# Performance work log

Measured on AMD Instinct MI355X. Metric: run time of the kernel, lower is better.

## Reference

```python
import jax, jax.numpy as jnp
import numpy as np

UNITS = 1024
HEADS = 16
DEPTH = UNITS // HEADS          # 64
REL_LEN = 64 + 1                # max_relative_position + 1
M = 2 * REL_LEN - 1             # 129 relative buckets (bidirectional)
B, L = 4, 1024


def setup_inputs() -> dict:
    key = jax.random.key(0)
    ks = jax.random.split(key, 8)
    s = 0.02
    x = jax.random.normal(ks[0], (B, L, UNITS), jnp.float32)
    wq = jax.random.normal(ks[1], (UNITS, UNITS), jnp.float32) * s
    wk = jax.random.normal(ks[2], (UNITS, UNITS), jnp.float32) * s
    wv = jax.random.normal(ks[3], (UNITS, UNITS), jnp.float32) * s
    wo = jax.random.normal(ks[4], (UNITS, UNITS), jnp.float32) * s
    bo = jnp.zeros((UNITS,), jnp.float32)
    ek = jax.random.normal(ks[5], (HEADS, M, DEPTH), jnp.float32) * s
    ev = jax.random.normal(ks[6], (HEADS, M, DEPTH), jnp.float32) * s
    pad_mask = jnp.zeros((B, 1, 1, L), jnp.float32)  # 1.0 where padded
    return dict(x=x, pad_mask=pad_mask, wq=wq, wk=wk, wv=wv, wo=wo, bo=bo, ek=ek, ev=ev)


def _rel_idx(length):
    # relative offset j - i, clipped to [-(REL_LEN-1), REL_LEN-1], shifted to [0, M-1].
    # Equivalent to the pad/reshape/slice skew trick: padding_relative_embeddings tiles the
    # edge embeddings (== clipping) and relative_to_absolute_pos realizes idx = j - i + REL_LEN - 1.
    i = jnp.arange(length)
    off = i[None, :] - i[:, None]
    return jnp.clip(off, -(REL_LEN - 1), REL_LEN - 1) + (REL_LEN - 1)  # [L, L] int32


def _forward(x, pad_mask, wq, wk, wv, wo, bo, ek, ev):
    b, length, _ = x.shape

    def split_heads(h):  # [B, L, U] -> [B, H, L, D]
        return jnp.transpose(h.reshape(b, length, HEADS, DEPTH), (0, 2, 1, 3))

    q = split_heads(x @ wq)
    k = split_heads(x @ wk)
    v = split_heads(x @ wv)

    idx = _rel_idx(length)                                   # [L, L]
    qk = jnp.einsum('bhid,bhjd->bhij', q, k)                 # [B, H, L, L]
    # relative key logits: q . E_k over relative buckets, then relative->absolute gather
    qm = jnp.einsum('bhld,hmd->bhlm', q, ek)                 # [B, H, L, M]
    rel_k = jnp.take_along_axis(qm, idx[None, None, :, :], axis=-1)  # [B, H, L, L]
    logits = (qk + rel_k) / jnp.sqrt(jnp.asarray(DEPTH, jnp.float32))
    logits = logits + pad_mask * -1e9
    attn = jax.nn.softmax(logits, axis=-1)                   # [B, H, L, L]
    out = jnp.einsum('bhij,bhjd->bhid', attn, v)             # [B, H, L, D]

    # value relative position: out[b,h,i,d] += sum_j attn[b,h,i,j] * E_v[h, idx[i,j], d]
    # Implemented by scattering attn into relative buckets (avoids the [H,L,L,D] tensor
    # the original materializes), mathematically identical.
    def per_query(attn_i, idx_i):  # attn_i [B, H, L], idx_i [L]
        return jax.ops.segment_sum(jnp.moveaxis(attn_i, -1, 0), idx_i, num_segments=M)  # [M, B, H]

    wr = jax.vmap(per_query, in_axes=(2, 0))(attn, idx)      # [L, M, B, H]
    wr = jnp.transpose(wr, (2, 3, 0, 1))                     # [B, H, L, M]
    out = out + jnp.einsum('bhlm,hmd->bhld', wr, ev)

    out = jnp.transpose(out, (0, 2, 1, 3)).reshape(b, length, UNITS)  # combine heads
    return out @ wo + bo


def reference(x, pad_mask, wq, wk, wv, wo, bo, ek, ev):
    return _forward(x, pad_mask, wq, wk, wv, wo, bo, ek, ev)
```

## Files before the change

kernel.cpp:

```cpp
#include <hip/hip_runtime.h>

typedef unsigned short u16;
typedef short s16x8 __attribute__((ext_vector_type(8)));
typedef float f32x4 __attribute__((ext_vector_type(4)));

static __device__ __forceinline__ u16 f2b(float f) {
  union { float f; unsigned u; } v; v.f = f;
  unsigned r = v.u + 0x7fffu + ((v.u >> 16) & 1u);
  return (u16)(r >> 16);
}
static __device__ __forceinline__ float b2f(u16 u) {
  union { unsigned u; float f; } v; v.u = ((unsigned)u) << 16;
  return v.f;
}

#define MFMA16(a, b, c) __builtin_amdgcn_mfma_f32_16x16x32_bf16((a), (b), (c), 0, 0, 0)

static __device__ __forceinline__ void gload_lds16(const u16* g, u16* l) {
  __builtin_amdgcn_global_load_lds((const __attribute__((address_space(1))) void*)g,
                                   (__attribute__((address_space(3))) void*)l, 16, 0, 0);
}

__global__ void k_cast_x(const float* __restrict__ src, u16* __restrict__ dst, int n4) {
  int i = blockIdx.x * blockDim.x + threadIdx.x;
  if (i >= n4) return;
  float4 v = ((const float4*)src)[i];
  ushort4 o;
  o.x = f2b(v.x); o.y = f2b(v.y); o.z = f2b(v.z); o.w = f2b(v.w);
  ((ushort4*)dst)[i] = o;
}

__global__ void k_transpose_w(const float* wq, const float* wk, const float* wv, const float* wo,
                              u16* dq, u16* dk, u16* dv, u16* dwo) {
  const float* src; u16* dst;
  int z = blockIdx.z;
  if (z == 0)      { src = wq; dst = dq; }
  else if (z == 1) { src = wk; dst = dk; }
  else if (z == 2) { src = wv; dst = dv; }
  else             { src = wo; dst = dwo; }
  __shared__ float t[32][33];
  int x0 = blockIdx.x * 32, y0 = blockIdx.y * 32;
  int tx = threadIdx.x, ty = threadIdx.y;
#pragma unroll
  for (int k = 0; k < 4; k++) t[ty + 8 * k][tx] = src[(size_t)(y0 + ty + 8 * k) * 1024 + x0 + tx];
  __syncthreads();
#pragma unroll
  for (int k = 0; k < 4; k++) dst[(size_t)(x0 + ty + 8 * k) * 1024 + y0 + tx] = f2b(t[tx][ty + 8 * k]);
}

__global__ void k_prep_rel(const float* __restrict__ ek, const float* __restrict__ ev,
                           u16* __restrict__ ekb, u16* __restrict__ evt) {
  int i = blockIdx.x * blockDim.x + threadIdx.x;
  if (i < 16 * 144 * 64) {
    int h = i / (144 * 64); int rem = i % (144 * 64); int m = rem / 64; int d = rem % 64;
    ekb[i] = (m < 129) ? f2b(ek[((size_t)h * 129 + m) * 64 + d]) : (u16)0;
  }
  if (i < 16 * 64 * 160) {
    int h = i / (64 * 160); int rem = i % (64 * 160); int d = rem / 160; int mm = rem % 160;
    evt[i] = (mm < 129) ? f2b(ev[((size_t)h * 129 + mm) * 64 + d]) : (u16)0;
  }
}

template <int MODE>
static __device__ __forceinline__ void gemm_body(const u16* __restrict__ A, const u16* __restrict__ Bt,
                                                 void* __restrict__ Cout, const float* __restrict__ bias,
                                                 int bx, int by) {
  __shared__ u16 As[128 * 32];
  __shared__ u16 Bs[128 * 32];
  int tid = threadIdx.x;
  int w = tid >> 6, lane = tid & 63;
  int wrw = w >> 1, wcw = w & 1, lr = lane & 15, lk = lane >> 4;
  int m0 = by * 128, n0 = bx * 128;
  f32x4 acc[4][4] = {};
  int crow = lane >> 2;
  int ccol = (lane & 3) * 8;
  const u16* gA = &A [(size_t)(m0 + w * 32 + crow) * 1024 + ccol];
  const u16* gB = &Bt[(size_t)(n0 + w * 32 + crow) * 1024 + ccol];
  u16* lA = &As[w * 32 * 32];
  u16* lB = &Bs[w * 32 * 32];
  for (int k0 = 0; k0 < 1024; k0 += 32) {
    __syncthreads();
    gload_lds16(gA + k0,             lA);
    gload_lds16(gA + k0 + 16 * 1024, lA + 16 * 32);
    gload_lds16(gB + k0,             lB);
    gload_lds16(gB + k0 + 16 * 1024, lB + 16 * 32);
    __syncthreads();
    s16x8 af[4], bfr[4];
#pragma unroll
    for (int mt = 0; mt < 4; mt++) af[mt]  = *(const s16x8*)&As[(wrw * 64 + mt * 16 + lr) * 32 + lk * 8];
#pragma unroll
    for (int nt = 0; nt < 4; nt++) bfr[nt] = *(const s16x8*)&Bs[(wcw * 64 + nt * 16 + lr) * 32 + lk * 8];
    __builtin_amdgcn_s_setprio(1);
#pragma unroll
    for (int mt = 0; mt < 4; mt++)
#pragma unroll
      for (int nt = 0; nt < 4; nt++) {
        if (MODE == 1) acc[mt][nt] = MFMA16(bfr[nt], af[mt], acc[mt][nt]);
        else           acc[mt][nt] = MFMA16(af[mt], bfr[nt], acc[mt][nt]);
      }
    __builtin_amdgcn_s_setprio(0);
  }
#pragma unroll
  for (int mt = 0; mt < 4; mt++)
#pragma unroll
    for (int nt = 0; nt < 4; nt++)
#pragma unroll
      for (int r = 0; r < 4; r++) {
        float v = acc[mt][nt][r];
        if (MODE == 1) {
          int u = n0 + wcw * 64 + nt * 16 + lk * 4 + r;
          int l = m0 + wrw * 64 + mt * 16 + lr;
          int bb = l >> 10, ll = l & 1023;
          int hh = u >> 6, dd = u & 63;
          ((u16*)Cout)[((size_t)(bb * 16 + hh)) * 65536 + (size_t)dd * 1024 + ll] = f2b(v);
        } else {
          int row = m0 + wrw * 64 + mt * 16 + lk * 4 + r;
          int col = n0 + wcw * 64 + nt * 16 + lr;
          if (MODE == 2) {
            ((float*)Cout)[(size_t)row * 1024 + col] = v + bias[col];
          } else {
            int bb = row >> 10, l = row & 1023;
            int hh = col >> 6, dd = col & 63;
            ((u16*)Cout)[((size_t)(bb * 16 + hh)) * 65536 + (size_t)l * 64 + dd] = f2b(v);
          }
        }
      }
}

__global__ __launch_bounds__(256) void k_gemm_qk(const u16* __restrict__ A,
                                                 const u16* __restrict__ BtQ, const u16* __restrict__ BtK,
                                                 u16* __restrict__ Qo, u16* __restrict__ Ko) {
  const u16* Bt = blockIdx.z ? BtK : BtQ;
  u16* C        = blockIdx.z ? Ko  : Qo;
  gemm_body<0>(A, Bt, C, nullptr, blockIdx.x, blockIdx.y);
}
__global__ __launch_bounds__(256) void k_gemm_v(const u16* __restrict__ A, const u16* __restrict__ Bt,
                                                u16* __restrict__ Vo) {
  gemm_body<1>(A, Bt, Vo, nullptr, blockIdx.x, blockIdx.y);
}
__global__ __launch_bounds__(256) void k_gemm_out(const u16* __restrict__ A, const u16* __restrict__ Bt,
                                                  float* __restrict__ Cout, const float* __restrict__ bias) {
  gemm_body<2>(A, Bt, Cout, bias, blockIdx.x, blockIdx.y);
}

__global__ __launch_bounds__(64) void k_attn(const u16* __restrict__ Qg, const u16* __restrict__ Kg,
                                             const u16* __restrict__ Vt, const u16* __restrict__ ekb,
                                             const u16* __restrict__ evt, const float* __restrict__ pmask,
                                             u16* __restrict__ Og) {
  __shared__ alignas(16) char smem[16128];
  u16* qm_s   = (u16*)smem;
  u16* P_s    = (u16*)(smem + 4352);
  u16* wrb    = (u16*)(smem + 8704);
  u16* mask_s = (u16*)(smem + 14080);

  int lane = threadIdx.x;
  int lr = lane & 15, lk = lane >> 4;
  int wg = (blockIdx.x & 7) * 512 + (blockIdx.x >> 3);
  int bh = wg >> 6, it = wg & 63;
  int b = bh >> 4, h = bh & 15;
  int i0 = it * 16;

  {
    const float4* pm4 = (const float4*)(pmask + (size_t)b * 1024);
#pragma unroll
    for (int t = 0; t < 4; t++) {
      float4 v = pm4[lane * 4 + t];
      unsigned w0 = (unsigned)f2b(v.x * -1e9f) | ((unsigned)f2b(v.y * -1e9f) << 16);
      unsigned w1 = (unsigned)f2b(v.z * -1e9f) | ((unsigned)f2b(v.w * -1e9f) << 16);
      ((unsigned*)mask_s)[lane * 8 + t * 2]     = w0;
      ((unsigned*)mask_s)[lane * 8 + t * 2 + 1] = w1;
    }
  }
  for (int t = lane; t < 1344; t += 64) ((unsigned*)wrb)[t] = 0u;

  const u16* qp = &Qg[((size_t)bh * 1024 + i0 + lr) * 64 + lk * 8];
  s16x8 aq0 = *(const s16x8*)qp;
  s16x8 aq1 = *(const s16x8*)(qp + 32);

#pragma unroll
  for (int nt = 0; nt < 9; nt++) {
    f32x4 c = {};
    const u16* ekp = &ekb[((size_t)h * 144 + nt * 16 + lr) * 64 + lk * 8];
    c = MFMA16(aq0, *(const s16x8*)ekp, c);
    c = MFMA16(aq1, *(const s16x8*)(ekp + 32), c);
    int mcol = nt * 16 + lr;
    if (mcol < 129) {
#pragma unroll
      for (int r = 0; r < 4; r++) qm_s[(lk * 4 + r) * 136 + mcol] = f2b(c[r]);
    }
  }

  float ssum = 0.f, lsum = 0.f, rsum = 0.f;
  f32x4 oacc[4] = {};
  const int ig = i0 + lr;

  for (int jt = 0; jt < 8; jt++) {
    int j0 = jt * 128;
    float p[8][4];
    const u16* kbase = &Kg[((size_t)bh * 1024 + j0 + lr) * 64 + lk * 8];
#pragma unroll
    for (int nt = 0; nt < 8; nt++) {
      f32x4 c = {};
      const u16* kp = kbase + nt * 16 * 64;
      c = MFMA16(*(const s16x8*)kp, aq0, c);
      c = MFMA16(*(const s16x8*)(kp + 32), aq1, c);
#pragma unroll
      for (int r = 0; r < 4; r++) {
        int j = j0 + nt * 16 + lk * 4 + r;
        int dl = j - ig;
        dl = dl < -64 ? -64 : (dl > 64 ? 64 : dl);
        float qmv = b2f(qm_s[lr * 136 + dl + 64]);
        float madd = b2f(mask_s[j]);
        float sval = fminf((c[r] + qmv) * 0.125f + madd, 80.f);
        float pv = __expf(sval);
        p[nt][r] = pv;
        ssum += pv;
      }
    }
#pragma unroll
    for (int nt = 0; nt < 8; nt++) {
      unsigned lo, hi;
      asm("v_cvt_pk_bf16_f32 %0, %1, %2" : "=v"(lo) : "v"(p[nt][0]), "v"(p[nt][1]));
      asm("v_cvt_pk_bf16_f32 %0, %1, %2" : "=v"(hi) : "v"(p[nt][2]), "v"(p[nt][3]));
      uint2 pk; pk.x = lo; pk.y = hi;
      *(uint2*)&P_s[lr * 136 + nt * 16 + lk * 4] = pk;
    }
    __builtin_amdgcn_s_setprio(1);
    {
      s16x8 ap[4];
#pragma unroll
      for (int kk = 0; kk < 4; kk++) ap[kk] = *(const s16x8*)&P_s[lr * 136 + kk * 32 + lk * 8];
      const u16* vbase = &Vt[((size_t)bh * 64 + lr) * 1024 + j0 + lk * 8];
#pragma unroll
      for (int nt = 0; nt < 4; nt++) {
        const u16* vp = vbase + nt * 16 * 1024;
#pragma unroll
        for (int kk = 0; kk < 4; kk++)
          oacc[nt] = MFMA16(ap[kk], *(const s16x8*)(vp + kk * 32), oacc[nt]);
      }
    }
    __builtin_amdgcn_s_setprio(0);
    {
      int jmin = j0 + lk * 4;
      int jmax = j0 + 112 + lk * 4 + 3;
      if (jmax <= ig - 64) {
        float s = 0.f;
#pragma unroll
        for (int nt = 0; nt < 8; nt++) s += (p[nt][0] + p[nt][1]) + (p[nt][2] + p[nt][3]);
        lsum += s;
      } else if (jmin >= ig + 64) {
        float s = 0.f;
#pragma unroll
        for (int nt = 0; nt < 8; nt++) s += (p[nt][0] + p[nt][1]) + (p[nt][2] + p[nt][3]);
        rsum += s;
      } else {
#pragma unroll
        for (int nt = 0; nt < 8; nt++)
#pragma unroll
          for (int r = 0; r < 4; r++) {
            int dl = j0 + nt * 16 + lk * 4 + r - ig;
            if (dl <= -64) lsum += p[nt][r];
            else if (dl >= 64) rsum += p[nt][r];
            else wrb[lr * 168 + dl + 64] = f2b(p[nt][r]);
          }
      }
    }
  }

  lsum += __shfl_xor(lsum, 16); lsum += __shfl_xor(lsum, 32);
  rsum += __shfl_xor(rsum, 16); rsum += __shfl_xor(rsum, 32);
  ssum += __shfl_xor(ssum, 16); ssum += __shfl_xor(ssum, 32);
  if (lk == 0) {
    wrb[lr * 168]       = f2b(lsum);
    wrb[lr * 168 + 128] = f2b(rsum);
  }

  __builtin_amdgcn_s_setprio(1);
  {
    s16x8 aw[5];
#pragma unroll
    for (int kk = 0; kk < 5; kk++) aw[kk] = *(const s16x8*)&wrb[lr * 168 + kk * 32 + lk * 8];
    const u16* ebase = &evt[((size_t)h * 64 + lr) * 160 + lk * 8];
#pragma unroll
    for (int nt = 0; nt < 4; nt++) {
      const u16* ep = ebase + nt * 16 * 160;
#pragma unroll
      for (int kk = 0; kk < 5; kk++)
        oacc[nt] = MFMA16(aw[kk], *(const s16x8*)(ep + kk * 32), oacc[nt]);
    }
  }
  __builtin_amdgcn_s_setprio(0);

  float rden[4];
#pragma unroll
  for (int r = 0; r < 4; r++) rden[r] = 1.0f / __shfl(ssum, lk * 4 + r);
  u16* obase = &Og[((size_t)(b * 1024 + i0)) * 1024 + h * 64];
#pragma unroll
  for (int nt = 0; nt < 4; nt++)
#pragma unroll
    for (int r = 0; r < 4; r++) {
      int il = lk * 4 + r;
      obase[(size_t)il * 1024 + nt * 16 + lr] = f2b(oacc[nt][r] * rden[r]);
    }
}

#define OFF_XB   0u
#define OFF_WQT  8388608u
#define OFF_WKT  10485760u
#define OFF_WVT  12582912u
#define OFF_WOT  14680064u
#define OFF_Q    16777216u
#define OFF_K    25165824u
#define OFF_VT   33554432u
#define OFF_O    41943040u
#define OFF_EKB  50331648u
#define OFF_EVT  50626560u

extern "C" void kernel_launch(void* const* d_in, const int* in_sizes, int n_in,
                              void* d_out, int out_size, void* d_ws, size_t ws_size,
                              hipStream_t stream) {
  const float* x  = (const float*)d_in[0];
  const float* pm = (const float*)d_in[1];
  const float* wq = (const float*)d_in[2];
  const float* wk = (const float*)d_in[3];
  const float* wv = (const float*)d_in[4];
  const float* wo = (const float*)d_in[5];
  const float* bo = (const float*)d_in[6];
  const float* ek = (const float*)d_in[7];
  const float* ev = (const float*)d_in[8];
  char* ws = (char*)d_ws;
  u16* Xb  = (u16*)(ws + OFF_XB);
  u16* Wqt = (u16*)(ws + OFF_WQT);
  u16* Wkt = (u16*)(ws + OFF_WKT);
  u16* Wvt = (u16*)(ws + OFF_WVT);
  u16* Wot = (u16*)(ws + OFF_WOT);
  u16* Qg  = (u16*)(ws + OFF_Q);
  u16* Kg  = (u16*)(ws + OFF_K);
  u16* Vtg = (u16*)(ws + OFF_VT);
  u16* Og  = (u16*)(ws + OFF_O);
  u16* EKB = (u16*)(ws + OFF_EKB);
  u16* EVT = (u16*)(ws + OFF_EVT);

  k_cast_x<<<4096, 256, 0, stream>>>(x, Xb, 1048576);
  {
    dim3 tb(32, 8), tg(32, 32, 4);
    k_transpose_w<<<tg, tb, 0, stream>>>(wq, wk, wv, wo, Wqt, Wkt, Wvt, Wot);
  }
  k_prep_rel<<<640, 256, 0, stream>>>(ek, ev, EKB, EVT);
  {
    dim3 gqk(8, 32, 2);
    k_gemm_qk<<<gqk, 256, 0, stream>>>(Xb, Wqt, Wkt, Qg, Kg);
    dim3 gv(8, 32);
    k_gemm_v<<<gv, 256, 0, stream>>>(Xb, Wvt, Vtg);
    k_attn<<<4096, 64, 0, stream>>>(Qg, Kg, Vtg, EKB, EVT, pm, Og);
    dim3 go(8, 32);
    k_gemm_out<<<go, 256, 0, stream>>>(Og, Wot, (float*)d_out, bo);
  }
}
```

Before: 319.7 us.

## Specialize attention tiles by relative region, fold scale into Q, double-buffer GEMM

Attention key tiles are split into left-clipped, diagonal and right-clipped classes, so the far tiles skip the per-element relative-logit lookups and bucket scatter and use a single per-row clipped value. The softmax scale and log2(e) are folded into the Q projection output so the kernel can use a raw hardware exp2. The pad mask is precomputed once in bf16 instead of per block. The right-edge value bucket is applied as a scalar FMA instead of an extra MFMA K-step. The projection GEMMs gain double-buffered LDS loads. The costs are more code paths and extra bf16 rounding of the scaled Q.

After: 338.2 us. 1.06x slower.

```diff
diff --git a/kernel.cpp b/kernel.cpp
--- a/kernel.cpp
+++ b/kernel.cpp
@@ -3,6 +3,9 @@
 typedef unsigned short u16;
 typedef short s16x8 __attribute__((ext_vector_type(8)));
 typedef float f32x4 __attribute__((ext_vector_type(4)));
+
+#define ALPHA 0.18033688f
+#define MASKC -1.44269504e9f
 
 static __device__ __forceinline__ u16 f2b(float f) {
   union { float f; unsigned u; } v; v.f = f;
@@ -12,6 +15,9 @@
 static __device__ __forceinline__ float b2f(u16 u) {
   union { unsigned u; float f; } v; v.u = ((unsigned)u) << 16;
   return v.f;
+}
+static __device__ __forceinline__ float exp2_hw(float x) {
+  float r; asm("v_exp_f32 %0, %1" : "=v"(r) : "v"(x)); return r;
 }
 
 #define MFMA16(a, b, c) __builtin_amdgcn_mfma_f32_16x16x32_bf16((a), (b), (c), 0, 0, 0)
@@ -49,7 +55,8 @@
 }
 
 __global__ void k_prep_rel(const float* __restrict__ ek, const float* __restrict__ ev,
-                           u16* __restrict__ ekb, u16* __restrict__ evt) {
+                           const float* __restrict__ pm,
+                           u16* __restrict__ ekb, u16* __restrict__ evt, u16* __restrict__ maskb) {
   int i = blockIdx.x * blockDim.x + threadIdx.x;
   if (i < 16 * 144 * 64) {
     int h = i / (144 * 64); int rem = i % (144 * 64); int m = rem / 64; int d = rem % 64;
@@ -59,14 +66,15 @@
     int h = i / (64 * 160); int rem = i % (64 * 160); int d = rem / 160; int mm = rem % 160;
     evt[i] = (mm < 129) ? f2b(ev[((size_t)h * 129 + mm) * 64 + d]) : (u16)0;
   }
+  if (i < 4096) maskb[i] = f2b(pm[i] * MASKC);
 }
 
 template <int MODE>
 static __device__ __forceinline__ void gemm_body(const u16* __restrict__ A, const u16* __restrict__ Bt,
                                                  void* __restrict__ Cout, const float* __restrict__ bias,
-                                                 int bx, int by) {
-  __shared__ u16 As[128 * 32];
-  __shared__ u16 Bs[128 * 32];
+                                                 float oscale, int bx, int by) {
+  __shared__ u16 As[2][128 * 32];
+  __shared__ u16 Bs[2][128 * 32];
   int tid = threadIdx.x;
   int w = tid >> 6, lane = tid & 63;
   int wrw = w >> 1, wcw = w & 1, lr = lane & 15, lk = lane >> 4;
@@ -76,20 +84,26 @@
   int ccol = (lane & 3) * 8;
   const u16* gA = &A [(size_t)(m0 + w * 32 + crow) * 1024 + ccol];
   const u16* gB = &Bt[(size_t)(n0 + w * 32 + crow) * 1024 + ccol];
-  u16* lA = &As[w * 32 * 32];
-  u16* lB = &Bs[w * 32 * 32];
-  for (int k0 = 0; k0 < 1024; k0 += 32) {
-    __syncthreads();
+
+  auto STAGE = [&](int buf, int k0) {
+    u16* lA = &As[buf][w * 1024];
+    u16* lB = &Bs[buf][w * 1024];
     gload_lds16(gA + k0,             lA);
     gload_lds16(gA + k0 + 16 * 1024, lA + 16 * 32);
     gload_lds16(gB + k0,             lB);
     gload_lds16(gB + k0 + 16 * 1024, lB + 16 * 32);
-    __syncthreads();
+  };
+
+  STAGE(0, 0);
+  __syncthreads();
+  int cur = 0;
+  for (int t = 0; t < 32; t++) {
+    if (t < 31) STAGE(cur ^ 1, (t + 1) * 32);
     s16x8 af[4], bfr[4];
 #pragma unroll
-    for (int mt = 0; mt < 4; mt++) af[mt]  = *(const s16x8*)&As[(wrw * 64 + mt * 16 + lr) * 32 + lk * 8];
-#pragma unroll
-    for (int nt = 0; nt < 4; nt++) bfr[nt] = *(const s16x8*)&Bs[(wcw * 64 + nt * 16 + lr) * 32 + lk * 8];
+    for (int mt = 0; mt < 4; mt++) af[mt]  = *(const s16x8*)&As[cur][(wrw * 64 + mt * 16 + lr) * 32 + lk * 8];
+#pragma unroll
+    for (int nt = 0; nt < 4; nt++) bfr[nt] = *(const s16x8*)&Bs[cur][(wcw * 64 + nt * 16 + lr) * 32 + lk * 8];
     __builtin_amdgcn_s_setprio(1);
 #pragma unroll
     for (int mt = 0; mt < 4; mt++)
@@ -99,6 +113,8 @@
         else           acc[mt][nt] = MFMA16(af[mt], bfr[nt], acc[mt][nt]);
       }
     __builtin_amdgcn_s_setprio(0);
+    __syncthreads();
+    cur ^= 1;
   }
 #pragma unroll
   for (int mt = 0; mt < 4; mt++)
@@ -121,7 +137,7 @@
           } else {
             int bb = row >> 10, l = row & 1023;
             int hh = col >> 6, dd = col & 63;
-            ((u16*)Cout)[((size_t)(bb * 16 + hh)) * 65536 + (size_t)l * 64 + dd] = f2b(v);
+            ((u16*)Cout)[((size_t)(bb * 16 + hh)) * 65536 + (size_t)l * 64 + dd] = f2b(v * oscale);
           }
         }
       }
@@ -132,26 +148,101 @@
                                                  u16* __restrict__ Qo, u16* __restrict__ Ko) {
   const u16* Bt = blockIdx.z ? BtK : BtQ;
   u16* C        = blockIdx.z ? Ko  : Qo;
-  gemm_body<0>(A, Bt, C, nullptr, blockIdx.x, blockIdx.y);
+  gemm_body<0>(A, Bt, C, nullptr, blockIdx.z ? 1.0f : ALPHA, blockIdx.x, blockIdx.y);
 }
 __global__ __launch_bounds__(256) void k_gemm_v(const u16* __restrict__ A, const u16* __restrict__ Bt,
                                                 u16* __restrict__ Vo) {
-  gemm_body<1>(A, Bt, Vo, nullptr, blockIdx.x, blockIdx.y);
+  gemm_body<1>(A, Bt, Vo, nullptr, 1.0f, blockIdx.x, blockIdx.y);
 }
 __global__ __launch_bounds__(256) void k_gemm_out(const u16* __restrict__ A, const u16* __restrict__ Bt,
                                                   float* __restrict__ Cout, const float* __restrict__ bias) {
-  gemm_body<2>(A, Bt, Cout, bias, blockIdx.x, blockIdx.y);
+  gemm_body<2>(A, Bt, Cout, bias, 1.0f, blockIdx.x, blockIdx.y);
+}
+
+template <int CLS>
+static __device__ __forceinline__ void attn_tile(
+    int j0, const u16* __restrict__ Kt, const u16* __restrict__ Vt0, const u16* __restrict__ mrow,
+    s16x8 aq0, s16x8 aq1, u16* qm_s, u16* P_s, u16* wrb,
+    float qmL, float qmR, int lr, int lk, int ig,
+    f32x4 oacc[4], float& ssum, float& lsum, float& rsum)
+{
+  float p[8][4];
+  const u16* kbase = Kt + (size_t)(j0 + lr) * 64 + lk * 8;
+  const u16* mbase = &mrow[j0 + lk * 4];
+#pragma unroll
+  for (int nt = 0; nt < 8; nt++) {
+    f32x4 c = {};
+    const u16* kp = kbase + nt * 1024;
+    c = MFMA16(*(const s16x8*)kp, aq0, c);
+    c = MFMA16(*(const s16x8*)(kp + 32), aq1, c);
+    ushort4 mv = *(const ushort4*)(mbase + nt * 16);
+#pragma unroll
+    for (int r = 0; r < 4; r++) {
+      float qmv;
+      if (CLS == 0) qmv = qmL;
+      else if (CLS == 2) qmv = qmR;
+      else {
+        int dl = j0 + nt * 16 + lk * 4 + r - ig;
+        dl = dl < -64 ? -64 : (dl > 64 ? 64 : dl);
+        qmv = b2f(qm_s[lr * 136 + dl + 64]);
+      }
+      float mr = b2f(r == 0 ? mv.x : r == 1 ? mv.y : r == 2 ? mv.z : mv.w);
+      p[nt][r] = exp2_hw(fminf(c[r] + qmv + mr, 110.f));
+    }
+  }
+#pragma unroll
+  for (int nt = 0; nt < 8; nt++) {
+    unsigned lo, hi;
+    asm("v_cvt_pk_bf16_f32 %0, %1, %2" : "=v"(lo) : "v"(p[nt][0]), "v"(p[nt][1]));
+    asm("v_cvt_pk_bf16_f32 %0, %1, %2" : "=v"(hi) : "v"(p[nt][2]), "v"(p[nt][3]));
+    uint2 pk; pk.x = lo; pk.y = hi;
+    *(uint2*)&P_s[lr * 136 + nt * 16 + lk * 4] = pk;
+  }
+  __builtin_amdgcn_s_setprio(1);
+  {
+    s16x8 ap[4];
+#pragma unroll
+    for (int kk = 0; kk < 4; kk++) ap[kk] = *(const s16x8*)&P_s[lr * 136 + kk * 32 + lk * 8];
+    const u16* vbase = Vt0 + (size_t)lr * 1024 + j0 + lk * 8;
+#pragma unroll
+    for (int nt = 0; nt < 4; nt++) {
+      const u16* vp = vbase + nt * 16 * 1024;
+#pragma unroll
+      for (int kk = 0; kk < 4; kk++)
+        oacc[nt] = MFMA16(ap[kk], *(const s16x8*)(vp + kk * 32), oacc[nt]);
+    }
+  }
+  __builtin_amdgcn_s_setprio(0);
+  if (CLS != 1) {
+    float s01 = 0.f, s23 = 0.f;
+#pragma unroll
+    for (int nt = 0; nt < 8; nt++) { s01 += p[nt][0] + p[nt][1]; s23 += p[nt][2] + p[nt][3]; }
+    float s = s01 + s23;
+    ssum += s;
+    if (CLS == 0) lsum += s; else rsum += s;
+  } else {
+#pragma unroll
+    for (int nt = 0; nt < 8; nt++)
+#pragma unroll
+      for (int r = 0; r < 4; r++) {
+        float pv = p[nt][r];
+        ssum += pv;
+        int dl = j0 + nt * 16 + lk * 4 + r - ig;
+        if (dl <= -64) lsum += pv;
+        else if (dl >= 64) rsum += pv;
+        else wrb[lr * 136 + dl + 64] = f2b(pv);
+      }
+  }
 }
 
 __global__ __launch_bounds__(64) void k_attn(const u16* __restrict__ Qg, const u16* __restrict__ Kg,
                                              const u16* __restrict__ Vt, const u16* __restrict__ ekb,
-                                             const u16* __restrict__ evt, const float* __restrict__ pmask,
+                                             const u16* __restrict__ evt, const u16* __restrict__ maskb,
                                              u16* __restrict__ Og) {
-  __shared__ alignas(16) char smem[16128];
-  u16* qm_s   = (u16*)smem;
-  u16* P_s    = (u16*)(smem + 4352);
-  u16* wrb    = (u16*)(smem + 8704);
-  u16* mask_s = (u16*)(smem + 14080);
+  __shared__ alignas(16) char smem[13056];
+  u16* qm_s = (u16*)smem;
+  u16* P_s  = (u16*)(smem + 4352);
+  u16* wrb  = (u16*)(smem + 8704);
 
   int lane = threadIdx.x;
   int lr = lane & 15, lk = lane >> 4;
@@ -160,18 +251,7 @@
   int b = bh >> 4, h = bh & 15;
   int i0 = it * 16;
 
-  {
-    const float4* pm4 = (const float4*)(pmask + (size_t)b * 1024);
-#pragma unroll
-    for (int t = 0; t < 4; t++) {
-      float4 v = pm4[lane * 4 + t];
-      unsigned w0 = (unsigned)f2b(v.x * -1e9f) | ((unsigned)f2b(v.y * -1e9f) << 16);
-      unsigned w1 = (unsigned)f2b(v.z * -1e9f) | ((unsigned)f2b(v.w * -1e9f) << 16);
-      ((unsigned*)mask_s)[lane * 8 + t * 2]     = w0;
-      ((unsigned*)mask_s)[lane * 8 + t * 2 + 1] = w1;
-    }
-  }
-  for (int t = lane; t < 1344; t += 64) ((unsigned*)wrb)[t] = 0u;
+  for (int t = lane; t < 1088; t += 64) ((unsigned*)wrb)[t] = 0u;
 
   const u16* qp = &Qg[((size_t)bh * 1024 + i0 + lr) * 64 + lk * 8];
   s16x8 aq0 = *(const s16x8*)qp;
@@ -189,107 +269,57 @@
       for (int r = 0; r < 4; r++) qm_s[(lk * 4 + r) * 136 + mcol] = f2b(c[r]);
     }
   }
+  float qmL = b2f(qm_s[lr * 136]);
+  float qmR = b2f(qm_s[lr * 136 + 128]);
 
   float ssum = 0.f, lsum = 0.f, rsum = 0.f;
   f32x4 oacc[4] = {};
   const int ig = i0 + lr;
-
-  for (int jt = 0; jt < 8; jt++) {
-    int j0 = jt * 128;
-    float p[8][4];
-    const u16* kbase = &Kg[((size_t)bh * 1024 + j0 + lr) * 64 + lk * 8];
-#pragma unroll
-    for (int nt = 0; nt < 8; nt++) {
-      f32x4 c = {};
-      const u16* kp = kbase + nt * 16 * 64;
-      c = MFMA16(*(const s16x8*)kp, aq0, c);
-      c = MFMA16(*(const s16x8*)(kp + 32), aq1, c);
-#pragma unroll
-      for (int r = 0; r < 4; r++) {
-        int j = j0 + nt * 16 + lk * 4 + r;
-        int dl = j - ig;
-        dl = dl < -64 ? -64 : (dl > 64 ? 64 : dl);
-        float qmv = b2f(qm_s[lr * 136 + dl + 64]);
-        float madd = b2f(mask_s[j]);
-        float sval = fminf((c[r] + qmv) * 0.125f + madd, 80.f);
-        float pv = __expf(sval);
-        p[nt][r] = pv;
-        ssum += pv;
-      }
-    }
-#pragma unroll
-    for (int nt = 0; nt < 8; nt++) {
-      unsigned lo, hi;
-      asm("v_cvt_pk_bf16_f32 %0, %1, %2" : "=v"(lo) : "v"(p[nt][0]), "v"(p[nt][1]));
-      asm("v_cvt_pk_bf16_f32 %0, %1, %2" : "=v"(hi) : "v"(p[nt][2]), "v"(p[nt][3]));
-      uint2 pk; pk.x = lo; pk.y = hi;
-      *(uint2*)&P_s[lr * 136 + nt * 16 + lk * 4] = pk;
-    }
-    __builtin_amdgcn_s_setprio(1);
-    {
-      s16x8 ap[4];
-#pragma unroll
-      for (int kk = 0; kk < 4; kk++) ap[kk] = *(const s16x8*)&P_s[lr * 136 + kk * 32 + lk * 8];
-      const u16* vbase = &Vt[((size_t)bh * 64 + lr) * 1024 + j0 + lk * 8];
-#pragma unroll
-      for (int nt = 0; nt < 4; nt++) {
-        const u16* vp = vbase + nt * 16 * 1024;
-#pragma unroll
-        for (int kk = 0; kk < 4; kk++)
-          oacc[nt] = MFMA16(ap[kk], *(const s16x8*)(vp + kk * 32), oacc[nt]);
-      }
-    }
-    __builtin_amdgcn_s_setprio(0);
-    {
-      int jmin = j0 + lk * 4;
-      int jmax = j0 + 112 + lk * 4 + 3;
-      if (jmax <= ig - 64) {
-        float s = 0.f;
-#pragma unroll
-        for (int nt = 0; nt < 8; nt++) s += (p[nt][0] + p[nt][1]) + (p[nt][2] + p[nt][3]);
-        lsum += s;
-      } else if (jmin >= ig + 64) {
-        float s = 0.f;
-#pragma unroll
-        for (int nt = 0; nt < 8; nt++) s += (p[nt][0] + p[nt][1]) + (p[nt][2] + p[nt][3]);
-        rsum += s;
-      } else {
-#pragma unroll
-        for (int nt = 0; nt < 8; nt++)
-#pragma unroll
-          for (int r = 0; r < 4; r++) {
-            int dl = j0 + nt * 16 + lk * 4 + r - ig;
-            if (dl <= -64) lsum += p[nt][r];
-            else if (dl >= 64) rsum += p[nt][r];
-            else wrb[lr * 168 + dl + 64] = f2b(p[nt][r]);
-          }
-      }
-    }
-  }
+  const u16* Kt  = Kg + (size_t)bh * 65536;
+  const u16* Vt0 = Vt + (size_t)bh * 65536;
+  const u16* mrow = maskb + b * 1024;
+
+  int jtL = (i0 - 64) >> 7; if (jtL < 0) jtL = 0;
+  int jtR = (i0 + 207) >> 7; if (jtR > 8) jtR = 8;
+  for (int jt = 0; jt < jtL; jt++)
+    attn_tile<0>(jt * 128, Kt, Vt0, mrow, aq0, aq1, qm_s, P_s, wrb, qmL, qmR, lr, lk, ig, oacc, ssum, lsum, rsum);
+  for (int jt = jtL; jt < jtR; jt++)
+    attn_tile<1>(jt * 128, Kt, Vt0, mrow, aq0, aq1, qm_s, P_s, wrb, qmL, qmR, lr, lk, ig, oacc, ssum, lsum, rsum);
+  for (int jt = jtR; jt < 8; jt++)
+    attn_tile<2>(jt * 128, Kt, Vt0, mrow, aq0, aq1, qm_s, P_s, wrb, qmL, qmR, lr, lk, ig, oacc, ssum, lsum, rsum);
 
   lsum += __shfl_xor(lsum, 16); lsum += __shfl_xor(lsum, 32);
   rsum += __shfl_xor(rsum, 16); rsum += __shfl_xor(rsum, 32);
   ssum += __shfl_xor(ssum, 16); ssum += __shfl_xor(ssum, 32);
-  if (lk == 0) {
-    wrb[lr * 168]       = f2b(lsum);
-    wrb[lr * 168 + 128] = f2b(rsum);
-  }
+  if (lk == 0) wrb[lr * 136] = f2b(lsum);
 
   __builtin_amdgcn_s_setprio(1);
   {
-    s16x8 aw[5];
-#pragma unroll
-    for (int kk = 0; kk < 5; kk++) aw[kk] = *(const s16x8*)&wrb[lr * 168 + kk * 32 + lk * 8];
+    s16x8 aw[4];
+#pragma unroll
+    for (int kk = 0; kk < 4; kk++) aw[kk] = *(const s16x8*)&wrb[lr * 136 + kk * 32 + lk * 8];
     const u16* ebase = &evt[((size_t)h * 64 + lr) * 160 + lk * 8];
 #pragma unroll
     for (int nt = 0; nt < 4; nt++) {
       const u16* ep = ebase + nt * 16 * 160;
 #pragma unroll
-      for (int kk = 0; kk < 5; kk++)
+      for (int kk = 0; kk < 4; kk++)
         oacc[nt] = MFMA16(aw[kk], *(const s16x8*)(ep + kk * 32), oacc[nt]);
     }
   }
   __builtin_amdgcn_s_setprio(0);
+
+  {
+    float rs[4];
+#pragma unroll
+    for (int r = 0; r < 4; r++) rs[r] = __shfl(rsum, lk * 4 + r);
+#pragma unroll
+    for (int nt = 0; nt < 4; nt++) {
+      float evc = b2f(evt[((size_t)h * 64 + nt * 16 + lr) * 160 + 128]);
+#pragma unroll
+      for (int r = 0; r < 4; r++) oacc[nt][r] += rs[r] * evc;
+    }
+  }
 
   float rden[4];
 #pragma unroll
@@ -315,6 +345,7 @@
 #define OFF_O    41943040u
 #define OFF_EKB  50331648u
 #define OFF_EVT  50626560u
+#define OFF_MB   50954240u
 
 extern "C" void kernel_launch(void* const* d_in, const int* in_sizes, int n_in,
                               void* d_out, int out_size, void* d_ws, size_t ws_size,
@@ -340,19 +371,20 @@
   u16* Og  = (u16*)(ws + OFF_O);
   u16* EKB = (u16*)(ws + OFF_EKB);
   u16* EVT = (u16*)(ws + OFF_EVT);
+  u16* MB  = (u16*)(ws + OFF_MB);
 
   k_cast_x<<<4096, 256, 0, stream>>>(x, Xb, 1048576);
   {
     dim3 tb(32, 8), tg(32, 32, 4);
     k_transpose_w<<<tg, tb, 0, stream>>>(wq, wk, wv, wo, Wqt, Wkt, Wvt, Wot);
   }
-  k_prep_rel<<<640, 256, 0, stream>>>(ek, ev, EKB, EVT);
+  k_prep_rel<<<640, 256, 0, stream>>>(ek, ev, pm, EKB, EVT, MB);
   {
     dim3 gqk(8, 32, 2);
     k_gemm_qk<<<gqk, 256, 0, stream>>>(Xb, Wqt, Wkt, Qg, Kg);
     dim3 gv(8, 32);
     k_gemm_v<<<gv, 256, 0, stream>>>(Xb, Wvt, Vtg);
-    k_attn<<<4096, 64, 0, stream>>>(Qg, Kg, Vtg, EKB, EVT, pm, Og);
+    k_attn<<<4096, 64, 0, stream>>>(Qg, Kg, Vtg, EKB, EVT, MB, Og);
     dim3 go(8, 32);
     k_gemm_out<<<go, 256, 0, stream>>>(Og, Wot, (float*)d_out, bo);
   }
```
